# Kernel optimization log

Measured on AMD Instinct MI355X. Metric: run time of the kernel, lower is better.

## Reference

```python
import jax, jax.numpy as jnp
import numpy as np

N_NODES = 10000
N_EDGES = 20000
N_GRAPHS = 64
DIM = 64
NFEAT = 32
EDIM = 16
NCLS = 10
EPS = 1e-5  # BatchNorm eps (torch default)


def setup_inputs() -> dict:
    key = jax.random.key(0)
    ks = jax.random.split(key, 20)
    def w(k, shape, s=0.05):
        return jax.random.normal(k, shape, dtype=jnp.float32) * s
    z = lambda *s: jnp.zeros(s, jnp.float32)
    inp = {}
    inp["x"] = jax.random.normal(ks[0], (N_NODES, NFEAT), dtype=jnp.float32)
    inp["edge_index"] = jax.random.randint(ks[1], (2, N_EDGES), 0, N_NODES)
    inp["edge_attr"] = jax.random.normal(ks[2], (N_EDGES, EDIM), dtype=jnp.float32)
    inp["batch"] = jax.random.randint(ks[3], (N_NODES,), 0, N_GRAPHS)
    # edge_transform
    inp["et_w"] = w(ks[4], (EDIM, DIM)); inp["et_b"] = z(DIM)
    # conv_in edge-MLP (dim->128->num_features*dim) + root weight + bias
    inp["nn1_w1"] = w(ks[5], (DIM, 128)); inp["nn1_b1"] = z(128)
    inp["nn1_w2"] = w(ks[6], (128, NFEAT * DIM)); inp["nn1_b2"] = z(NFEAT * DIM)
    inp["root_in"] = w(ks[7], (NFEAT, DIM)); inp["bias_in"] = z(DIM)
    # 4 residual NNConv layers, params stacked on leading axis
    inp["convs_w1"] = w(ks[8], (4, DIM, 128)); inp["convs_b1"] = z(4, 128)
    inp["convs_w2"] = w(ks[9], (4, 128, DIM * DIM)); inp["convs_b2"] = z(4, DIM * DIM)
    inp["convs_root"] = w(ks[10], (4, DIM, DIM)); inp["convs_bias"] = z(4, DIM)
    # 5 BatchNorm layers (affine)
    inp["bn_gamma"] = jnp.ones((5, DIM), jnp.float32); inp["bn_beta"] = z(5, DIM)
    # head
    inp["lin1_w"] = w(ks[11], (DIM, DIM)); inp["lin1_b"] = z(DIM)
    inp["lin2_w"] = w(ks[12], (DIM, DIM)); inp["lin2_b"] = z(DIM)
    inp["lout_w"] = w(ks[13], (DIM, NCLS)); inp["lout_b"] = z(NCLS)
    return inp


def _bn(x, g, b):
    # BatchNorm1d training-mode math: biased variance over nodes
    m = x.mean(0)
    v = jnp.mean((x - m) ** 2, 0)
    return g * (x - m) / jnp.sqrt(v + EPS) + b


def _nnconv(x, src, dst, e, w1, b1, w2, b2, root, bias, in_dim):
    # PyG NNConv: per-edge weight matrix from edge MLP, gather->bmm->scatter-add, plus root transform
    h = jax.nn.relu(e @ w1 + b1)                       # [E,128]
    W = (h @ w2 + b2).reshape(-1, in_dim, DIM)         # [E,in,out]
    msg = jnp.einsum('ei,eio->eo', x[src], W)          # [E,out]
    agg = jax.ops.segment_sum(msg, dst, num_segments=N_NODES)
    return agg + x @ root + bias


def reference(x, edge_index, edge_attr, batch,
              et_w, et_b,
              nn1_w1, nn1_b1, nn1_w2, nn1_b2, root_in, bias_in,
              convs_w1, convs_b1, convs_w2, convs_b2, convs_root, convs_bias,
              bn_gamma, bn_beta,
              lin1_w, lin1_b, lin2_w, lin2_b, lout_w, lout_b):
    src, dst = edge_index[0], edge_index[1]
    e = edge_attr @ et_w + et_b                        # [E,DIM]
    h = jax.nn.relu(_bn(
        _nnconv(x, src, dst, e, nn1_w1, nn1_b1, nn1_w2, nn1_b2, root_in, bias_in, NFEAT),
        bn_gamma[0], bn_beta[0]))
    for k in range(4):  # residual NNConv blocks
        h = jax.nn.relu(_bn(
            _nnconv(h, src, dst, e, convs_w1[k], convs_b1[k], convs_w2[k], convs_b2[k],
                    convs_root[k], convs_bias[k], DIM),
            bn_gamma[k + 1], bn_beta[k + 1])) + h
    g = jax.ops.segment_max(h, batch, num_segments=N_GRAPHS)  # global_max_pool
    g = jax.nn.relu(g @ lin1_w + lin1_b)  # dropout = identity (eval/deterministic)
    g = jax.nn.relu(g @ lin2_w + lin2_b)
    return jax.nn.sigmoid(g @ lout_w + lout_b)
```

## Files before the change

### kernel.cpp

```cpp
#include <hip/hip_runtime.h>
#include <hip/hip_bf16.h>
#include <math.h>

#define N_NODES 10000
#define N_EDGES 20000
#define EPAD 20224
#define N_GRAPHS 64
#define DIM 64
#define NFEAT 32
#define EDIM 16
#define NCLS 10

static_assert(EPAD == 79 * 256, "EPAD");

typedef short short8 __attribute__((ext_vector_type(8)));
typedef float f32x16 __attribute__((ext_vector_type(16)));

static __device__ __forceinline__ short f2b(float f) {
  __hip_bfloat16 h = __float2bfloat16(f);
  return __builtin_bit_cast(short, h);
}

static __device__ __forceinline__ void gload_lds16(const void* g, void* s) {
  __builtin_amdgcn_global_load_lds(
      (const __attribute__((address_space(1))) unsigned int*)g,
      (__attribute__((address_space(3))) unsigned int*)s, 16, 0, 0);
}

__global__ __launch_bounds__(256) void k_pre(
    const float* __restrict__ ea, const float* __restrict__ etw,
    const float* __restrict__ etb, const float* __restrict__ nw1,
    const float* __restrict__ nb1, const float* __restrict__ x,
    const float* __restrict__ rootw, const float* __restrict__ rootb,
    const float* __restrict__ w20, const float* __restrict__ b20,
    const float* __restrict__ w2c, const float* __restrict__ b2c,
    float* __restrict__ h1T, float* __restrict__ agg,
    double* __restrict__ part0, short* __restrict__ pk,
    float* __restrict__ gpool) {
  const int b = blockIdx.x, t = threadIdx.x;
  if (b < 1161) {
    if (b == 0) { for (int i = t; i < N_GRAPHS * DIM; i += 256) gpool[i] = 0.f; }
    __shared__ float tile[32][65];
    const float *w2, *b2; short* out; int K, lb;
    if (b < 129) { w2 = w20; b2 = b20; out = pk; K = 4096; lb = b; }
    else {
      int bb = b - 129; int k = bb / 258; lb = bb % 258;
      w2 = w2c + (size_t)k * 8192 * 64; b2 = b2c + (size_t)k * 4096;
      out = pk + 264192 + (size_t)k * 528384; K = 8192;
    }
    #pragma unroll
    for (int it = 0; it < 2; ++it) {
      int idx = t + it * 256;
      int r = idx >> 4, c4 = idx & 15;
      int k = lb * 32 + r;
      const float* sp = (k < K) ? (w2 + (size_t)k * 64 + c4 * 4)
                                : (b2 + (size_t)(k - K) * 64 + c4 * 4);
      float4 v = *(const float4*)sp;
      float* dr = &tile[r][c4 * 4];
      dr[0] = v.x; dr[1] = v.y; dr[2] = v.z; dr[3] = v.w;
    }
    __syncthreads();
    const int S_local = t >> 7, n = (t >> 6) & 1, l = t & 63;
    const int rbase = S_local * 16 + ((l >> 5) << 3);
    const int col = n * 32 + (l & 31);
    short8 o;
    #pragma unroll
    for (int u = 0; u < 8; ++u) o[u] = f2b(tile[rbase + u][col]);
    ((short8*)out)[(size_t)lb * 256 + t] = o;
  } else if (b < 3661) {
    const int e0 = (b - 1161) * 8;
    __shared__ float sea[8][17];
    __shared__ float se[8][65];
    if (t < 128) {
      int r = t >> 4, c = t & 15;
      sea[r][c] = ea[(size_t)(e0 + r) * EDIM + c];
    }
    __syncthreads();
    {
      int o = t & 63, eh = t >> 6;
      #pragma unroll
      for (int k = 0; k < 2; ++k) {
        int r = eh * 2 + k;
        float a = etb[o];
        #pragma unroll
        for (int i = 0; i < EDIM; ++i) a = fmaf(sea[r][i], etw[i * 64 + o], a);
        se[r][o] = a;
      }
    }
    __syncthreads();
    {
      int j = t & 127, eh = t >> 7;
      int r0 = eh * 4;
      float a0 = nb1[j], a1 = a0, a2 = a0, a3 = a0;
      #pragma unroll 8
      for (int i = 0; i < 64; ++i) {
        float wv = nw1[i * 128 + j];
        a0 = fmaf(se[r0 + 0][i], wv, a0);
        a1 = fmaf(se[r0 + 1][i], wv, a1);
        a2 = fmaf(se[r0 + 2][i], wv, a2);
        a3 = fmaf(se[r0 + 3][i], wv, a3);
      }
      float4 o = {fmaxf(a0, 0.f), fmaxf(a1, 0.f), fmaxf(a2, 0.f), fmaxf(a3, 0.f)};
      *(float4*)(h1T + (size_t)j * EPAD + e0 + r0) = o;
    }
  } else {
    const int u = b - 3661;
    if (u == 0 && t < 128) part0[t] = 0.0;
    int idx = u * 256 + t;
    if (idx < N_NODES * DIM) {
      int n = idx >> 6, o = idx & 63;
      float a = rootb[o];
      const float* hr = x + (size_t)n * NFEAT;
      #pragma unroll 8
      for (int i = 0; i < NFEAT; ++i) a = fmaf(hr[i], rootw[i * 64 + o], a);
      agg[idx] = a;
    }
  }
}

template<int IN, int NC>
__global__ __launch_bounds__(256, 2) void k_msg(
    const float* __restrict__ h1T, const float* __restrict__ xin,
    const int* __restrict__ src, const short* __restrict__ pk,
    float* __restrict__ pt) {
  constexpr int QW = IN / 16;
  constexpr int JR = 128 / NC;
  constexpr int GB = QW * 2048;
  __shared__ float sh_h[256][JR + 1];
  __shared__ __align__(16) short bbuf[3][QW * 1024];
  const int t = threadIdx.x, l = t & 63, w = t >> 6;
  const int e0 = blockIdx.x * 256;
  const int jbase = blockIdx.y * JR;
  const int ng = JR + (blockIdx.y == 0 ? 1 : 0);

  const char* pkc = (const char*)pk;
  const char* bias_gb = pkc + (size_t)(8 * IN) * 2048;

  auto stage = [&](int g) {
    const char* gb = (g < JR) ? pkc + (size_t)(jbase + g) * GB : bias_gb;
    #pragma unroll
    for (int s = 0; s < QW / 2; ++s) {
      int off = w * (QW * 512) + s * 1024;
      gload_lds16(gb + off + l * 16, (char*)&bbuf[g % 3][0] + off);
    }
  };

  #pragma unroll
  for (int it = 0; it < JR / 4; ++it) {
    int u = t + it * 256;
    int jj = u >> 6, c4 = u & 63;
    float4 v = *(const float4*)(h1T + (size_t)(jbase + jj) * EPAD + e0 + c4 * 4);
    sh_h[c4 * 4 + 0][jj] = v.x;
    sh_h[c4 * 4 + 1][jj] = v.y;
    sh_h[c4 * 4 + 2][jj] = v.z;
    sh_h[c4 * 4 + 3][jj] = v.w;
  }

  const int h8 = (l >> 5) << 3;
  float xr[2][QW][8];
  #pragma unroll
  for (int m = 0; m < 2; ++m) {
    int eme = e0 + w * 64 + m * 32 + (l & 31);
    int srow = src[eme < N_EDGES ? eme : 0];
    #pragma unroll
    for (int q = 0; q < QW; ++q) {
      const float* xp = xin + (size_t)srow * IN + q * 16 + h8;
      float4 a = *(const float4*)xp;
      float4 bq = *(const float4*)(xp + 4);
      xr[m][q][0] = a.x;  xr[m][q][1] = a.y;  xr[m][q][2] = a.z;  xr[m][q][3] = a.w;
      xr[m][q][4] = bq.x; xr[m][q][5] = bq.y; xr[m][q][6] = bq.z; xr[m][q][7] = bq.w;
    }
  }

  asm volatile("s_waitcnt vmcnt(0) lgkmcnt(0)" ::: "memory");
  stage(0);
  if (ng > 1) stage(1);

  f32x16 acc00 = {}, acc01 = {}, acc10 = {}, acc11 = {};

  for (int g = 0; g < ng; ++g) {
    if (g + 1 < ng) {
      if constexpr (QW / 2 == 2) asm volatile("s_waitcnt vmcnt(2)" ::: "memory");
      else                       asm volatile("s_waitcnt vmcnt(1)" ::: "memory");
    } else {
      asm volatile("s_waitcnt vmcnt(0)" ::: "memory");
    }
    asm volatile("s_barrier" ::: "memory");
    if (g + 2 < ng) stage(g + 2);
    const short8* bp = (const short8*)&bbuf[g % 3][0];
    if (g < JR) {
      float hv0 = sh_h[w * 64 + (l & 31)][g];
      float hv1 = sh_h[w * 64 + 32 + (l & 31)][g];
      #pragma unroll
      for (int q = 0; q < QW; ++q) {
        short8 b0 = bp[q * 128 + l];
        short8 b1 = bp[q * 128 + 64 + l];
        short8 av0, av1;
        #pragma unroll
        for (int u = 0; u < 8; ++u) {
          av0[u] = f2b(hv0 * xr[0][q][u]);
          av1[u] = f2b(hv1 * xr[1][q][u]);
        }
        acc00 = __builtin_amdgcn_mfma_f32_32x32x16_bf16(av0, b0, acc00, 0, 0, 0);
        acc01 = __builtin_amdgcn_mfma_f32_32x32x16_bf16(av0, b1, acc01, 0, 0, 0);
        acc10 = __builtin_amdgcn_mfma_f32_32x32x16_bf16(av1, b0, acc10, 0, 0, 0);
        acc11 = __builtin_amdgcn_mfma_f32_32x32x16_bf16(av1, b1, acc11, 0, 0, 0);
      }
    } else {
      #pragma unroll
      for (int q = 0; q < QW; ++q) {
        short8 b0 = bp[q * 128 + l];
        short8 b1 = bp[q * 128 + 64 + l];
        short8 av0, av1;
        #pragma unroll
        for (int u = 0; u < 8; ++u) {
          av0[u] = f2b(xr[0][q][u]);
          av1[u] = f2b(xr[1][q][u]);
        }
        acc00 = __builtin_amdgcn_mfma_f32_32x32x16_bf16(av0, b0, acc00, 0, 0, 0);
        acc01 = __builtin_amdgcn_mfma_f32_32x32x16_bf16(av0, b1, acc01, 0, 0, 0);
        acc10 = __builtin_amdgcn_mfma_f32_32x32x16_bf16(av1, b0, acc10, 0, 0, 0);
        acc11 = __builtin_amdgcn_mfma_f32_32x32x16_bf16(av1, b1, acc11, 0, 0, 0);
      }
    }
  }

  float* po = pt + ((size_t)blockIdx.y * EPAD + e0 + w * 64) * 64 + (l & 31);
  #pragma unroll
  for (int v = 0; v < 16; ++v) {
    int r = (v & 3) + ((v >> 2) << 3) + ((l >> 5) << 2);
    po[(size_t)r * 64]             = acc00[v];
    po[(size_t)r * 64 + 32]        = acc01[v];
    po[(size_t)(r + 32) * 64]      = acc10[v];
    po[(size_t)(r + 32) * 64 + 32] = acc11[v];
  }
}

__global__ __launch_bounds__(256) void k_reduce(const float* __restrict__ pt,
    const int* __restrict__ dst, float* __restrict__ agg) {
  int idx = blockIdx.x * 256 + threadIdx.x;
  int e = idx >> 4;
  if (e >= N_EDGES) return;
  int c = (idx & 15) << 2;
  const float* p = pt + (size_t)e * 64 + c;
  float4 a = *(const float4*)p;
  #pragma unroll
  for (int s = 1; s < 8; ++s) {
    float4 b = *(const float4*)(p + (size_t)s * EPAD * 64);
    a.x += b.x; a.y += b.y; a.z += b.z; a.w += b.w;
  }
  float* ap = agg + (size_t)dst[e] * 64 + c;
  atomicAdd(ap + 0, a.x);
  atomicAdd(ap + 1, a.y);
  atomicAdd(ap + 2, a.z);
  atomicAdd(ap + 3, a.w);
}

__global__ __launch_bounds__(256) void k_bnpart(const float* __restrict__ agg,
    double* __restrict__ part) {
  const int t = threadIdx.x;
  const int c = t & 63, rg = t >> 6;
  const int r0 = blockIdx.x * 50;
  const int r1 = min(r0 + 50, N_NODES);
  double s = 0.0, s2 = 0.0;
  for (int r = r0 + rg; r < r1; r += 4) {
    float v = agg[(size_t)r * 64 + c];
    s += v;
    s2 += (double)v * v;
  }
  __shared__ double shs[4][64];
  __shared__ double shq[4][64];
  shs[rg][c] = s; shq[rg][c] = s2;
  __syncthreads();
  if (t < 64) {
    double ts = shs[0][t] + shs[1][t] + shs[2][t] + shs[3][t];
    double tq = shq[0][t] + shq[1][t] + shq[2][t] + shq[3][t];
    atomicAdd(&part[t], ts);
    atomicAdd(&part[64 + t], tq);
  }
}

__global__ __launch_bounds__(256) void k_inter(
    float* __restrict__ agg, const double* __restrict__ part,
    const float* __restrict__ gamma, const float* __restrict__ beta,
    const float* resid, float* __restrict__ h_cur,
    const float* __restrict__ rootw, const float* __restrict__ rootb,
    double* __restrict__ partn,
    const float* __restrict__ ea, const float* __restrict__ etw,
    const float* __restrict__ etb, const float* __restrict__ w1,
    const float* __restrict__ b1, float* __restrict__ h1T) {
  const int b = blockIdx.x, t = threadIdx.x;
  if (b < 157) {
    __shared__ float sh[64][65];
    if (b == 0 && t < 128) partn[t] = 0.0;
    const int o = t & 63, rg = t >> 6;
    const int n0 = b * 64;
    float m = (float)(part[o] * (1.0 / N_NODES));
    float s2 = (float)(part[64 + o] * (1.0 / N_NODES));
    float inv = 1.0f / sqrtf(s2 - m * m + 1e-5f);
    float sc = gamma[o] * inv;
    float sf = beta[o] - m * sc;
    #pragma unroll
    for (int k = 0; k < 16; ++k) {
      int r = rg * 16 + k;
      int n = n0 + r;
      float v = 0.f;
      if (n < N_NODES) {
        v = fmaxf(fmaf(agg[(size_t)n * 64 + o], sc, sf), 0.f);
        if (resid) v += resid[(size_t)n * 64 + o];
        h_cur[(size_t)n * 64 + o] = v;
      }
      sh[r][o] = v;
    }
    __syncthreads();
    float acc[16];
    float rb = rootb[o];
    #pragma unroll
    for (int k = 0; k < 16; ++k) acc[k] = rb;
    for (int i = 0; i < 64; ++i) {
      float wv = rootw[i * 64 + o];
      #pragma unroll
      for (int k = 0; k < 16; ++k) acc[k] = fmaf(sh[rg * 16 + k][i], wv, acc[k]);
    }
    #pragma unroll
    for (int k = 0; k < 16; ++k) {
      int n = n0 + rg * 16 + k;
      if (n < N_NODES) agg[(size_t)n * 64 + o] = acc[k];
    }
  } else {
    const int e0 = (b - 157) * 8;
    __shared__ float sea[8][17];
    __shared__ float se[8][65];
    if (t < 128) {
      int r = t >> 4, c = t & 15;
      sea[r][c] = ea[(size_t)(e0 + r) * EDIM + c];
    }
    __syncthreads();
    {
      int o = t & 63, eh = t >> 6;
      #pragma unroll
      for (int k = 0; k < 2; ++k) {
        int r = eh * 2 + k;
        float a = etb[o];
        #pragma unroll
        for (int i = 0; i < EDIM; ++i) a = fmaf(sea[r][i], etw[i * 64 + o], a);
        se[r][o] = a;
      }
    }
    __syncthreads();
    {
      int j = t & 127, eh = t >> 7;
      int r0 = eh * 4;
      float a0 = b1[j], a1 = a0, a2 = a0, a3 = a0;
      #pragma unroll 8
      for (int i = 0; i < 64; ++i) {
        float wv = w1[i * 128 + j];
        a0 = fmaf(se[r0 + 0][i], wv, a0);
        a1 = fmaf(se[r0 + 1][i], wv, a1);
        a2 = fmaf(se[r0 + 2][i], wv, a2);
        a3 = fmaf(se[r0 + 3][i], wv, a3);
      }
      float4 o = {fmaxf(a0, 0.f), fmaxf(a1, 0.f), fmaxf(a2, 0.f), fmaxf(a3, 0.f)};
      *(float4*)(h1T + (size_t)j * EPAD + e0 + r0) = o;
    }
  }
}

__global__ __launch_bounds__(256) void k_final(const float* __restrict__ agg,
    const double* __restrict__ part, const float* __restrict__ gamma,
    const float* __restrict__ beta, const float* __restrict__ resid,
    const int* __restrict__ batch, float* __restrict__ gpool) {
  int idx = blockIdx.x * 256 + threadIdx.x;
  if (idx >= N_NODES * DIM) return;
  int c = idx & 63, r = idx >> 6;
  float m = (float)(part[c] * (1.0 / N_NODES));
  float s2 = (float)(part[64 + c] * (1.0 / N_NODES));
  float inv = 1.0f / sqrtf(s2 - m * m + 1e-5f);
  float sc = gamma[c] * inv;
  float sf = beta[c] - m * sc;
  float v = fmaxf(fmaf(agg[idx], sc, sf), 0.f) + resid[idx];
  atomicMax((unsigned int*)&gpool[batch[r] * 64 + c], __float_as_uint(v));
}

__global__ __launch_bounds__(64) void k_head(const float* __restrict__ g,
    const float* __restrict__ w1, const float* __restrict__ b1,
    const float* __restrict__ w2, const float* __restrict__ b2,
    const float* __restrict__ wo, const float* __restrict__ bo,
    float* __restrict__ out) {
  __shared__ float s0[64];
  __shared__ float s1[64];
  const int r = blockIdx.x, t = threadIdx.x;
  s0[t] = g[r * 64 + t];
  __syncthreads();
  float a = b1[t];
  #pragma unroll 8
  for (int i = 0; i < 64; ++i) a = fmaf(s0[i], w1[i * 64 + t], a);
  s1[t] = fmaxf(a, 0.f);
  __syncthreads();
  a = b2[t];
  #pragma unroll 8
  for (int i = 0; i < 64; ++i) a = fmaf(s1[i], w2[i * 64 + t], a);
  __syncthreads();
  s0[t] = fmaxf(a, 0.f);
  __syncthreads();
  if (t < NCLS) {
    float o = bo[t];
    #pragma unroll 8
    for (int i = 0; i < 64; ++i) o = fmaf(s0[i], wo[i * NCLS + t], o);
    out[r * NCLS + t] = 1.f / (1.f + expf(-o));
  }
}

extern "C" void kernel_launch(void* const* d_in, const int* in_sizes, int n_in,
                              void* d_out, int out_size, void* d_ws, size_t ws_size,
                              hipStream_t stream) {
  const float* x          = (const float*)d_in[0];
  const int*   eidx       = (const int*)d_in[1];
  const float* eattr      = (const float*)d_in[2];
  const int*   batch      = (const int*)d_in[3];
  const float* et_w       = (const float*)d_in[4];
  const float* et_b       = (const float*)d_in[5];
  const float* nn1_w1     = (const float*)d_in[6];
  const float* nn1_b1     = (const float*)d_in[7];
  const float* nn1_w2     = (const float*)d_in[8];
  const float* nn1_b2     = (const float*)d_in[9];
  const float* root_in    = (const float*)d_in[10];
  const float* bias_in    = (const float*)d_in[11];
  const float* convs_w1   = (const float*)d_in[12];
  const float* convs_b1   = (const float*)d_in[13];
  const float* convs_w2   = (const float*)d_in[14];
  const float* convs_b2   = (const float*)d_in[15];
  const float* convs_root = (const float*)d_in[16];
  const float* convs_bias = (const float*)d_in[17];
  const float* bn_gamma   = (const float*)d_in[18];
  const float* bn_beta    = (const float*)d_in[19];
  const float* lin1_w     = (const float*)d_in[20];
  const float* lin1_b     = (const float*)d_in[21];
  const float* lin2_w     = (const float*)d_in[22];
  const float* lin2_b     = (const float*)d_in[23];
  const float* lout_w     = (const float*)d_in[24];
  const float* lout_b     = (const float*)d_in[25];

  const int* srcp = eidx;
  const int* dstp = eidx + N_EDGES;

  char* wsb = (char*)d_ws;
  double* part0 = (double*)wsb;
  double* part1 = (double*)(wsb + 1024);
  float* h1T    = (float*)(wsb + 4096);
  float* agg    = h1T + 128 * EPAD;
  float* h_cur  = agg + N_NODES * 64;
  float* g      = h_cur + N_NODES * 64;
  short* pk0    = (short*)(g + N_GRAPHS * 64);
  short* pkL[4];
  for (int k = 0; k < 4; ++k) pkL[k] = pk0 + 264192 + (size_t)k * 528384;
  float* pt     = (float*)(pk0 + 264192 + 4 * 528384);
  double* parts[2] = {part0, part1};

  k_pre<<<6161, 256, 0, stream>>>(eattr, et_w, et_b, nn1_w1, nn1_b1, x,
                                  root_in, bias_in, nn1_w2, nn1_b2,
                                  convs_w2, convs_b2, h1T, agg, part0, pk0, g);

  k_msg<32, 8><<<dim3(79, 8), 256, 0, stream>>>(h1T, x, srcp, pk0, pt);
  k_reduce<<<(EPAD * 16) / 256, 256, 0, stream>>>(pt, dstp, agg);
  k_bnpart<<<200, 256, 0, stream>>>(agg, part0);

  for (int k = 0; k < 4; ++k) {
    k_inter<<<2657, 256, 0, stream>>>(
        agg, parts[k & 1], bn_gamma + k * 64, bn_beta + k * 64,
        (k == 0) ? nullptr : h_cur, h_cur,
        convs_root + (size_t)k * 4096, convs_bias + (size_t)k * 64,
        parts[(k + 1) & 1],
        eattr, et_w, et_b,
        convs_w1 + (size_t)k * 8192, convs_b1 + (size_t)k * 128, h1T);
    k_msg<64, 8><<<dim3(79, 8), 256, 0, stream>>>(h1T, h_cur, srcp, pkL[k], pt);
    k_reduce<<<(EPAD * 16) / 256, 256, 0, stream>>>(pt, dstp, agg);
    k_bnpart<<<200, 256, 0, stream>>>(agg, parts[(k + 1) & 1]);
  }

  k_final<<<2500, 256, 0, stream>>>(agg, parts[0], bn_gamma + 4 * 64,
                                    bn_beta + 4 * 64, h_cur, batch, g);
  k_head<<<N_GRAPHS, 64, 0, stream>>>(g, lin1_w, lin1_b, lin2_w, lin2_b,
                                      lout_w, lout_b, (float*)d_out);
}
```

Before: 449.7 us.

## Halve edges per message block to raise occupancy and grid size

The message kernel now gives each block 128 edges instead of 256. Each wave handles 32 edges with two accumulators instead of four, and the grid doubles to 158x8. The per-edge h buffer is transposed so it can be filled with float4 stores, and launch bounds now ask for 4 blocks per CU to cut register pressure and hide latency better. In exchange, each staged weight tile from LDS is reused across half as many edges, so total weight traffic into LDS doubles.

```diff
diff --git a/kernel.cpp b/kernel.cpp
--- a/kernel.cpp
+++ b/kernel.cpp
@@ -11,7 +11,7 @@
 #define EDIM 16
 #define NCLS 10
 
-static_assert(EPAD == 79 * 256, "EPAD");
+static_assert(EPAD == 158 * 128, "EPAD");
 
 typedef short short8 __attribute__((ext_vector_type(8)));
 typedef float f32x16 __attribute__((ext_vector_type(16)));
@@ -119,17 +119,17 @@
 }
 
 template<int IN, int NC>
-__global__ __launch_bounds__(256, 2) void k_msg(
+__global__ __launch_bounds__(256, 4) void k_msg(
     const float* __restrict__ h1T, const float* __restrict__ xin,
     const int* __restrict__ src, const short* __restrict__ pk,
     float* __restrict__ pt) {
   constexpr int QW = IN / 16;
   constexpr int JR = 128 / NC;
   constexpr int GB = QW * 2048;
-  __shared__ float sh_h[256][JR + 1];
+  __shared__ float sh_h[JR][128];
   __shared__ __align__(16) short bbuf[3][QW * 1024];
   const int t = threadIdx.x, l = t & 63, w = t >> 6;
-  const int e0 = blockIdx.x * 256;
+  const int e0 = blockIdx.x * 128;
   const int jbase = blockIdx.y * JR;
   const int ng = JR + (blockIdx.y == 0 ? 1 : 0);
 
@@ -146,37 +146,31 @@
   };
 
   #pragma unroll
-  for (int it = 0; it < JR / 4; ++it) {
+  for (int it = 0; it < (JR * 128) / 1024; ++it) {
     int u = t + it * 256;
-    int jj = u >> 6, c4 = u & 63;
+    int jj = u >> 5, c4 = u & 31;
     float4 v = *(const float4*)(h1T + (size_t)(jbase + jj) * EPAD + e0 + c4 * 4);
-    sh_h[c4 * 4 + 0][jj] = v.x;
-    sh_h[c4 * 4 + 1][jj] = v.y;
-    sh_h[c4 * 4 + 2][jj] = v.z;
-    sh_h[c4 * 4 + 3][jj] = v.w;
+    *(float4*)&sh_h[jj][c4 * 4] = v;
   }
 
   const int h8 = (l >> 5) << 3;
-  float xr[2][QW][8];
+  const int eme = e0 + w * 32 + (l & 31);
+  const int srow = src[eme < N_EDGES ? eme : 0];
+  float xr[QW][8];
   #pragma unroll
-  for (int m = 0; m < 2; ++m) {
-    int eme = e0 + w * 64 + m * 32 + (l & 31);
-    int srow = src[eme < N_EDGES ? eme : 0];
-    #pragma unroll
-    for (int q = 0; q < QW; ++q) {
-      const float* xp = xin + (size_t)srow * IN + q * 16 + h8;
-      float4 a = *(const float4*)xp;
-      float4 bq = *(const float4*)(xp + 4);
-      xr[m][q][0] = a.x;  xr[m][q][1] = a.y;  xr[m][q][2] = a.z;  xr[m][q][3] = a.w;
-      xr[m][q][4] = bq.x; xr[m][q][5] = bq.y; xr[m][q][6] = bq.z; xr[m][q][7] = bq.w;
-    }
+  for (int q = 0; q < QW; ++q) {
+    const float* xp = xin + (size_t)srow * IN + q * 16 + h8;
+    float4 a = *(const float4*)xp;
+    float4 bq = *(const float4*)(xp + 4);
+    xr[q][0] = a.x;  xr[q][1] = a.y;  xr[q][2] = a.z;  xr[q][3] = a.w;
+    xr[q][4] = bq.x; xr[q][5] = bq.y; xr[q][6] = bq.z; xr[q][7] = bq.w;
   }
 
   asm volatile("s_waitcnt vmcnt(0) lgkmcnt(0)" ::: "memory");
   stage(0);
   if (ng > 1) stage(1);
 
-  f32x16 acc00 = {}, acc01 = {}, acc10 = {}, acc11 = {};
+  f32x16 acc0 = {}, acc1 = {};
 
   for (int g = 0; g < ng; ++g) {
     if (g + 1 < ng) {
@@ -189,50 +183,37 @@
     if (g + 2 < ng) stage(g + 2);
     const short8* bp = (const short8*)&bbuf[g % 3][0];
     if (g < JR) {
-      float hv0 = sh_h[w * 64 + (l & 31)][g];
-      float hv1 = sh_h[w * 64 + 32 + (l & 31)][g];
+      float hv = sh_h[g][w * 32 + (l & 31)];
       #pragma unroll
       for (int q = 0; q < QW; ++q) {
         short8 b0 = bp[q * 128 + l];
         short8 b1 = bp[q * 128 + 64 + l];
-        short8 av0, av1;
+        short8 av;
         #pragma unroll
-        for (int u = 0; u < 8; ++u) {
-          av0[u] = f2b(hv0 * xr[0][q][u]);
-          av1[u] = f2b(hv1 * xr[1][q][u]);
-        }
-        acc00 = __builtin_amdgcn_mfma_f32_32x32x16_bf16(av0, b0, acc00, 0, 0, 0);
-        acc01 = __builtin_amdgcn_mfma_f32_32x32x16_bf16(av0, b1, acc01, 0, 0, 0);
-        acc10 = __builtin_amdgcn_mfma_f32_32x32x16_bf16(av1, b0, acc10, 0, 0, 0);
-        acc11 = __builtin_amdgcn_mfma_f32_32x32x16_bf16(av1, b1, acc11, 0, 0, 0);
+        for (int u = 0; u < 8; ++u) av[u] = f2b(hv * xr[q][u]);
+        acc0 = __builtin_amdgcn_mfma_f32_32x32x16_bf16(av, b0, acc0, 0, 0, 0);
+        acc1 = __builtin_amdgcn_mfma_f32_32x32x16_bf16(av, b1, acc1, 0, 0, 0);
       }
     } else {
       #pragma unroll
       for (int q = 0; q < QW; ++q) {
         short8 b0 = bp[q * 128 + l];
         short8 b1 = bp[q * 128 + 64 + l];
-        short8 av0, av1;
+        short8 av;
         #pragma unroll
-        for (int u = 0; u < 8; ++u) {
-          av0[u] = f2b(xr[0][q][u]);
-          av1[u] = f2b(xr[1][q][u]);
-        }
-        acc00 = __builtin_amdgcn_mfma_f32_32x32x16_bf16(av0, b0, acc00, 0, 0, 0);
-        acc01 = __builtin_amdgcn_mfma_f32_32x32x16_bf16(av0, b1, acc01, 0, 0, 0);
-        acc10 = __builtin_amdgcn_mfma_f32_32x32x16_bf16(av1, b0, acc10, 0, 0, 0);
-        acc11 = __builtin_amdgcn_mfma_f32_32x32x16_bf16(av1, b1, acc11, 0, 0, 0);
-      }
-    }
-  }
-
-  float* po = pt + ((size_t)blockIdx.y * EPAD + e0 + w * 64) * 64 + (l & 31);
+        for (int u = 0; u < 8; ++u) av[u] = f2b(xr[q][u]);
+        acc0 = __builtin_amdgcn_mfma_f32_32x32x16_bf16(av, b0, acc0, 0, 0, 0);
+        acc1 = __builtin_amdgcn_mfma_f32_32x32x16_bf16(av, b1, acc1, 0, 0, 0);
+      }
+    }
+  }
+
+  float* po = pt + ((size_t)blockIdx.y * EPAD + e0 + w * 32) * 64 + (l & 31);
   #pragma unroll
   for (int v = 0; v < 16; ++v) {
     int r = (v & 3) + ((v >> 2) << 3) + ((l >> 5) << 2);
-    po[(size_t)r * 64]             = acc00[v];
-    po[(size_t)r * 64 + 32]        = acc01[v];
-    po[(size_t)(r + 32) * 64]      = acc10[v];
-    po[(size_t)(r + 32) * 64 + 32] = acc11[v];
+    po[(size_t)r * 64]      = acc0[v];
+    po[(size_t)r * 64 + 32] = acc1[v];
   }
 }
 
@@ -461,7 +442,7 @@
                                   root_in, bias_in, nn1_w2, nn1_b2,
                                   convs_w2, convs_b2, h1T, agg, part0, pk0, g);
 
-  k_msg<32, 8><<<dim3(79, 8), 256, 0, stream>>>(h1T, x, srcp, pk0, pt);
+  k_msg<32, 8><<<dim3(158, 8), 256, 0, stream>>>(h1T, x, srcp, pk0, pt);
   k_reduce<<<(EPAD * 16) / 256, 256, 0, stream>>>(pt, dstp, agg);
   k_bnpart<<<200, 256, 0, stream>>>(agg, part0);
 
@@ -473,7 +454,7 @@
         parts[(k + 1) & 1],
         eattr, et_w, et_b,
         convs_w1 + (size_t)k * 8192, convs_b1 + (size_t)k * 128, h1T);
-    k_msg<64, 8><<<dim3(79, 8), 256, 0, stream>>>(h1T, h_cur, srcp, pkL[k], pt);
+    k_msg<64, 8><<<dim3(158, 8), 256, 0, stream>>>(h1T, h_cur, srcp, pkL[k], pt);
     k_reduce<<<(EPAD * 16) / 256, 256, 0, stream>>>(pt, dstp, agg);
     k_bnpart<<<200, 256, 0, stream>>>(agg, parts[(k + 1) & 1]);
   }
```

New measurement: 435.3 us. -3.2%, faster.

## Split message kernel into 16 j-chunks with bf16-packed partial outputs

Applied to the files above, without the earlier changes.

The per-edge message kernel now uses 16 hidden-unit chunks of 8 instead of 8 chunks of 16, which doubles the grid and raises the occupancy hint to 3 blocks per CU. Partial results are packed as bf16 pairs, so the partial buffer stays the same size even though there are twice as many slices. The reduce kernel now sums 16 bf16 slices per edge before the atomic scatter. The shared h tile is transposed so it can be written with float4 stores. The cost is extra bf16 rounding in the partial sums, plus more B-tile staging and twice the partial reads in the reduce.

```diff
diff --git a/kernel.cpp b/kernel.cpp
--- a/kernel.cpp
+++ b/kernel.cpp
@@ -19,6 +19,14 @@
 static __device__ __forceinline__ short f2b(float f) {
   __hip_bfloat16 h = __float2bfloat16(f);
   return __builtin_bit_cast(short, h);
+}
+static __device__ __forceinline__ unsigned pack2(float lo, float hi) {
+  return (unsigned)(unsigned short)f2b(lo) |
+         ((unsigned)(unsigned short)f2b(hi) << 16);
+}
+static __device__ __forceinline__ float b2f(unsigned short u) {
+  unsigned v = (unsigned)u << 16;
+  return __builtin_bit_cast(float, v);
 }
 
 static __device__ __forceinline__ void gload_lds16(const void* g, void* s) {
@@ -118,15 +126,15 @@
   }
 }
 
-template<int IN, int NC>
-__global__ __launch_bounds__(256, 2) void k_msg(
+template<int IN>
+__global__ __launch_bounds__(256, 3) void k_msg(
     const float* __restrict__ h1T, const float* __restrict__ xin,
     const int* __restrict__ src, const short* __restrict__ pk,
-    float* __restrict__ pt) {
+    unsigned* __restrict__ pt) {
   constexpr int QW = IN / 16;
-  constexpr int JR = 128 / NC;
+  constexpr int JR = 8;
   constexpr int GB = QW * 2048;
-  __shared__ float sh_h[256][JR + 1];
+  __shared__ float sh_h[JR][256];
   __shared__ __align__(16) short bbuf[3][QW * 1024];
   const int t = threadIdx.x, l = t & 63, w = t >> 6;
   const int e0 = blockIdx.x * 256;
@@ -146,14 +154,11 @@
   };
 
   #pragma unroll
-  for (int it = 0; it < JR / 4; ++it) {
+  for (int it = 0; it < 2; ++it) {
     int u = t + it * 256;
     int jj = u >> 6, c4 = u & 63;
     float4 v = *(const float4*)(h1T + (size_t)(jbase + jj) * EPAD + e0 + c4 * 4);
-    sh_h[c4 * 4 + 0][jj] = v.x;
-    sh_h[c4 * 4 + 1][jj] = v.y;
-    sh_h[c4 * 4 + 2][jj] = v.z;
-    sh_h[c4 * 4 + 3][jj] = v.w;
+    *(float4*)&sh_h[jj][c4 * 4] = v;
   }
 
   const int h8 = (l >> 5) << 3;
@@ -189,8 +194,8 @@
     if (g + 2 < ng) stage(g + 2);
     const short8* bp = (const short8*)&bbuf[g % 3][0];
     if (g < JR) {
-      float hv0 = sh_h[w * 64 + (l & 31)][g];
-      float hv1 = sh_h[w * 64 + 32 + (l & 31)][g];
+      float hv0 = sh_h[g][w * 64 + (l & 31)];
+      float hv1 = sh_h[g][w * 64 + 32 + (l & 31)];
       #pragma unroll
       for (int q = 0; q < QW; ++q) {
         short8 b0 = bp[q * 128 + l];
@@ -225,35 +230,36 @@
     }
   }
 
-  float* po = pt + ((size_t)blockIdx.y * EPAD + e0 + w * 64) * 64 + (l & 31);
+  unsigned* po = pt + ((size_t)blockIdx.y * EPAD + e0 + w * 64) * 32 + (l & 31);
   #pragma unroll
   for (int v = 0; v < 16; ++v) {
     int r = (v & 3) + ((v >> 2) << 3) + ((l >> 5) << 2);
-    po[(size_t)r * 64]             = acc00[v];
-    po[(size_t)r * 64 + 32]        = acc01[v];
-    po[(size_t)(r + 32) * 64]      = acc10[v];
-    po[(size_t)(r + 32) * 64 + 32] = acc11[v];
-  }
-}
-
-__global__ __launch_bounds__(256) void k_reduce(const float* __restrict__ pt,
+    po[(size_t)r * 32]        = pack2(acc00[v], acc01[v]);
+    po[(size_t)(r + 32) * 32] = pack2(acc10[v], acc11[v]);
+  }
+}
+
+__global__ __launch_bounds__(256) void k_reduce(const unsigned* __restrict__ pt,
     const int* __restrict__ dst, float* __restrict__ agg) {
   int idx = blockIdx.x * 256 + threadIdx.x;
-  int e = idx >> 4;
-  if (e >= N_EDGES) return;
-  int c = (idx & 15) << 2;
-  const float* p = pt + (size_t)e * 64 + c;
-  float4 a = *(const float4*)p;
+  int e = idx >> 3;
+  int w4 = (idx & 7) * 4;
+  const uint4* p = (const uint4*)(pt + (size_t)e * 32 + w4);
+  float lo[4] = {0.f, 0.f, 0.f, 0.f}, hi[4] = {0.f, 0.f, 0.f, 0.f};
   #pragma unroll
-  for (int s = 1; s < 8; ++s) {
-    float4 b = *(const float4*)(p + (size_t)s * EPAD * 64);
-    a.x += b.x; a.y += b.y; a.z += b.z; a.w += b.w;
-  }
-  float* ap = agg + (size_t)dst[e] * 64 + c;
-  atomicAdd(ap + 0, a.x);
-  atomicAdd(ap + 1, a.y);
-  atomicAdd(ap + 2, a.z);
-  atomicAdd(ap + 3, a.w);
+  for (int s = 0; s < 16; ++s) {
+    uint4 v = p[(size_t)s * EPAD * 8];
+    lo[0] += b2f((unsigned short)(v.x & 0xffff)); hi[0] += b2f((unsigned short)(v.x >> 16));
+    lo[1] += b2f((unsigned short)(v.y & 0xffff)); hi[1] += b2f((unsigned short)(v.y >> 16));
+    lo[2] += b2f((unsigned short)(v.z & 0xffff)); hi[2] += b2f((unsigned short)(v.z >> 16));
+    lo[3] += b2f((unsigned short)(v.w & 0xffff)); hi[3] += b2f((unsigned short)(v.w >> 16));
+  }
+  float* ap = agg + (size_t)dst[e] * 64 + w4;
+  #pragma unroll
+  for (int j = 0; j < 4; ++j) {
+    atomicAdd(ap + j, lo[j]);
+    atomicAdd(ap + 32 + j, hi[j]);
+  }
 }
 
 __global__ __launch_bounds__(256) void k_bnpart(const float* __restrict__ agg,
@@ -454,15 +460,15 @@
   short* pk0    = (short*)(g + N_GRAPHS * 64);
   short* pkL[4];
   for (int k = 0; k < 4; ++k) pkL[k] = pk0 + 264192 + (size_t)k * 528384;
-  float* pt     = (float*)(pk0 + 264192 + 4 * 528384);
+  unsigned* pt  = (unsigned*)(pk0 + 264192 + 4 * 528384);
   double* parts[2] = {part0, part1};
 
   k_pre<<<6161, 256, 0, stream>>>(eattr, et_w, et_b, nn1_w1, nn1_b1, x,
                                   root_in, bias_in, nn1_w2, nn1_b2,
                                   convs_w2, convs_b2, h1T, agg, part0, pk0, g);
 
-  k_msg<32, 8><<<dim3(79, 8), 256, 0, stream>>>(h1T, x, srcp, pk0, pt);
-  k_reduce<<<(EPAD * 16) / 256, 256, 0, stream>>>(pt, dstp, agg);
+  k_msg<32><<<dim3(79, 16), 256, 0, stream>>>(h1T, x, srcp, pk0, pt);
+  k_reduce<<<625, 256, 0, stream>>>(pt, dstp, agg);
   k_bnpart<<<200, 256, 0, stream>>>(agg, part0);
 
   for (int k = 0; k < 4; ++k) {
@@ -473,8 +479,8 @@
         parts[(k + 1) & 1],
         eattr, et_w, et_b,
         convs_w1 + (size_t)k * 8192, convs_b1 + (size_t)k * 128, h1T);
-    k_msg<64, 8><<<dim3(79, 8), 256, 0, stream>>>(h1T, h_cur, srcp, pkL[k], pt);
-    k_reduce<<<(EPAD * 16) / 256, 256, 0, stream>>>(pt, dstp, agg);
+    k_msg<64><<<dim3(79, 16), 256, 0, stream>>>(h1T, h_cur, srcp, pkL[k], pt);
+    k_reduce<<<625, 256, 0, stream>>>(pt, dstp, agg);
     k_bnpart<<<200, 256, 0, stream>>>(agg, parts[(k + 1) & 1]);
   }
 
```

Measured after the change: 640.8 us. +42.5%, slower.
